# Optimization experiments

Measured on AMD Instinct MI355X. Metric: run time of the kernel, lower is better.

The kernel has to match this reference:

```python
import jax, jax.numpy as jnp
import numpy as np

GRANULARITY = 50
PERCENTILES = (0.01, 0.99)


def setup_inputs() -> dict:
    key = jax.random.key(0)
    H = W = 6144
    sp = jax.random.uniform(key, (H, W), dtype=jnp.float32)
    return {
        "signal_probabilities": sp,
        "rho_max": jnp.float32(H - 1),
        "rho_min": jnp.float32(0.0),
        "theta_min_horizontal": jnp.float32(0.01),
        "theta_max_horizontal": jnp.float32(0.05),
        "theta_min_vertical": jnp.float32(1.52),
        "theta_max_vertical": jnp.float32(1.56),
    }


def _linspace(a, b, n):
    t = jnp.arange(n, dtype=jnp.float32) / (n - 1)
    return a + (b - a) * t


def _fix_edge_effects(buf):
    buf = buf.at[0, :].set(buf[1, :])
    buf = buf.at[-1, :].set(buf[-2, :])
    buf = buf.at[:, 0].set(buf[:, 1])
    buf = buf.at[:, -1].set(buf[:, -2])
    return buf


def _fill_buffer(H, W, thetas, rhos, mode):
    # vectorized over all granularity lines at once (no python loop over lines)
    if mode == "horizontal":
        y = jnp.arange(H)
        # x[g, H]: x = -y*tan(theta) + rho/cos(theta)
        x = -y[None, :] * jnp.tan(thetas)[:, None] + (rhos / jnp.cos(thetas))[:, None]
        x = jnp.clip(jnp.round(x).astype(jnp.int32), 0, W - 1)
        yb = jnp.broadcast_to(y[None, :], x.shape)
        buf = jnp.zeros((H, W), jnp.int32).at[yb, x].add(1)
        buf = jnp.cumsum(buf, axis=1)
    else:
        x = jnp.arange(W)
        # y[g, W]: y = -x/tan(theta) + rho/sin(theta)
        y = -x[None, :] / jnp.tan(thetas)[:, None] + (rhos / jnp.sin(thetas))[:, None]
        y = jnp.clip(jnp.round(y).astype(jnp.int32), 0, H - 1)
        xb = jnp.broadcast_to(x[None, :], y.shape)
        buf = jnp.zeros((H, W), jnp.int32).at[y, xb].add(1)
        buf = jnp.cumsum(buf, axis=0)
    return _fix_edge_effects(buf)


def _get_bounds(nsp, thetas, rhos, mode):
    g = GRANULARITY
    H, W = nsp.shape
    buf = _fill_buffer(H, W, thetas, rhos, mode)
    # segment-sum replaces the dense one_hot * probs reduction (same math)
    values = jax.ops.segment_sum(nsp.reshape(-1), buf.reshape(-1), num_segments=g)
    c = jnp.cumsum(values) / jnp.sum(values)
    lower = jnp.argmax(c >= PERCENTILES[0])  # first index with cumsum >= p0
    upper = (g - 1) - jnp.argmax((c <= PERCENTILES[1])[::-1]) + 2  # last index with cumsum <= p1, +2
    return lower, upper


def _take_neg(a, i):
    # a[-i] with python-style negative indexing (i == 0 -> a[0])
    g = a.shape[0]
    return jnp.take(a, (g - i) % g)


def _intersect(r1, t1, r2, t2):
    det = jnp.cos(t1) * jnp.sin(t2) - jnp.cos(t2) * jnp.sin(t1)
    x = (r1 * jnp.sin(t2) - r2 * jnp.sin(t1)) / det
    y = (r2 * jnp.cos(t1) - r1 * jnp.cos(t2)) / det
    return jnp.stack((x, y))


def reference(signal_probabilities, rho_max, rho_min, theta_min_horizontal,
              theta_max_horizontal, theta_min_vertical, theta_max_vertical):
    g = GRANULARITY
    nsp = signal_probabilities - signal_probabilities.min()
    nsp = nsp / nsp.sum()
    rhos = _linspace(rho_max, rho_min, g)
    th = _linspace(theta_min_horizontal, theta_max_horizontal, g)
    tv = _linspace(theta_min_vertical, theta_max_vertical, g)
    lh, uh = _get_bounds(nsp, th, rhos, "horizontal")
    lv, uv = _get_bounds(nsp, tv, rhos, "vertical")
    r_min_h, r_max_h = _take_neg(rhos, lh), _take_neg(rhos, uh)
    t_min_h, t_max_h = _take_neg(th, lh), _take_neg(th, uh)
    r_min_v, r_max_v = _take_neg(rhos, lv), _take_neg(rhos, uv)
    t_min_v, t_max_v = _take_neg(tv, lv), _take_neg(tv, uv)
    # [top-left, top-right, bottom-right, bottom-left] -> shape (4, 2)
    return jnp.stack([
        _intersect(r_min_h, t_min_h, r_min_v, t_min_v),
        _intersect(r_max_h, t_max_h, r_min_v, t_min_v),
        _intersect(r_max_h, t_max_h, r_max_v, t_max_v),
        _intersect(r_min_h, t_min_h, r_max_v, t_max_v),
    ], axis=0)
```

## Files before the change

kernel.cpp:

```cpp
#include <hip/hip_runtime.h>
#include <math.h>

#define HH 6144
#define WW 6144
constexpr int G = 50;
constexpr int NCOPY = 64;
constexpr int NG = NCOPY * G;
constexpr int BIG = 0x0FFFFFFF;
constexpr int MINBASE = 4 * NG;
constexpr int CTR = MINBASE + NCOPY;
constexpr int MASTER = CTR + NCOPY;
constexpr int C0 = MASTER + 2;

constexpr int TPB  = 384;
constexpr int PXT  = 16;
constexpr int NF4  = WW / 4;
constexpr int NBLK = HH;

__device__ inline void ldsAddF(float* p, float v)      { __hip_atomic_fetch_add(p, v, __ATOMIC_RELAXED, __HIP_MEMORY_SCOPE_WORKGROUP); }
__device__ inline void ldsAddU(unsigned* p, unsigned v){ __hip_atomic_fetch_add(p, v, __ATOMIC_RELAXED, __HIP_MEMORY_SCOPE_WORKGROUP); }
__device__ inline void glbAddF(float* p, float v)      { __hip_atomic_fetch_add(p, v, __ATOMIC_RELAXED, __HIP_MEMORY_SCOPE_AGENT); }
__device__ inline void glbAddU(unsigned* p, unsigned v){ __hip_atomic_fetch_add(p, v, __ATOMIC_RELAXED, __HIP_MEMORY_SCOPE_AGENT); }
__device__ inline unsigned glbAddCtr(unsigned* p)      { return __hip_atomic_fetch_add(p, 1u, __ATOMIC_RELAXED, __HIP_MEMORY_SCOPE_AGENT); }
__device__ inline float atomLoadF(const float* p)      { return __hip_atomic_load(p, __ATOMIC_RELAXED, __HIP_MEMORY_SCOPE_AGENT); }
__device__ inline unsigned atomLoadU(const unsigned* p){ return __hip_atomic_load(p, __ATOMIC_RELAXED, __HIP_MEMORY_SCOPE_AGENT); }

__global__ void crop_init(unsigned int* __restrict__ ws,
                          const float* __restrict__ p_rmax,
                          const float* __restrict__ p_rmin,
                          const float* __restrict__ p_thmin,
                          const float* __restrict__ p_thmax,
                          const float* __restrict__ p_tvmin,
                          const float* __restrict__ p_tvmax) {
  int i = blockIdx.x * 256 + threadIdx.x;
  if (i < MINBASE) ws[i] = 0u;
  else if (i < MINBASE + NCOPY) ws[i] = 0x7F800000u;
  else if (i < C0) ws[i] = 0u;

  if (blockIdx.x == 0 && threadIdx.x < G) {
    int t = threadIdx.x;
    double u    = (double)t / (double)(G - 1);
    double rmax = (double)p_rmax[0], rmin = (double)p_rmin[0];
    double rho  = rmax + (rmin - rmax) * u;
    double th   = (double)p_thmin[0] + ((double)p_thmax[0] - (double)p_thmin[0]) * u;
    double tv   = (double)p_tvmin[0] + ((double)p_tvmax[0] - (double)p_tvmin[0]) * u;
    double cth = cos(th), sth = sin(th);
    double ctv = cos(tv), stv = sin(tv);
    double* dT   = (double*)(ws + C0);
    double* dRC  = (double*)(ws + C0 + 100);
    float*  fva  = (float*)(ws + C0 + 200);
    float*  fvb  = (float*)(ws + C0 + 250);
    double* dRho = (double*)(ws + C0 + 300);
    double* dSth = (double*)(ws + C0 + 400);
    double* dCth = (double*)(ws + C0 + 500);
    double* dStv = (double*)(ws + C0 + 600);
    double* dCtv = (double*)(ws + C0 + 700);
    dT[t]  = tan(th);
    dRC[t] = rho / cth;
    fva[t] = (float)(rho / stv);
    fvb[t] = (float)(ctv / stv);
    dRho[t] = rho; dSth[t] = sth; dCth[t] = cth; dStv[t] = stv; dCtv[t] = ctv;
  }
}

__launch_bounds__(TPB)
__global__ void crop_main(const float* __restrict__ sp,
                          float* __restrict__ wsf,
                          float* __restrict__ out) {
  __shared__ float4 srow[NF4];
  __shared__ int pxh[G], pxv[G];
  __shared__ float hsum[G + 1], vsum[G + 1];
  __shared__ unsigned int hcnt[G + 1], vcnt[G + 1];
  __shared__ float wmin[TPB / 64];
  __shared__ int lastFlag;
  __shared__ double valS[100];
  __shared__ unsigned int valC[100];
  __shared__ float sminv;

  const int t  = threadIdx.x;
  const int y  = blockIdx.x;
  const int yp = min(max(y, 1), HH - 2);
  const float fyp = (float)yp;

  const float4* rowp = (const float4*)(sp + (size_t)y * WW);
  float4 a0 = rowp[t], a1 = rowp[t + 384], a2 = rowp[t + 768], a3 = rowp[t + 1152];

  for (int i = t; i < G + 1; i += TPB) { hsum[i] = 0.f; vsum[i] = 0.f; hcnt[i] = 0u; vcnt[i] = 0u; }

  const unsigned int* wsu = (const unsigned int*)wsf;
  if (t < G) {
    const double* dT  = (const double*)(wsu + C0);
    const double* dRC = (const double*)(wsu + C0 + 100);
    const float*  fva = (const float*)(wsu + C0 + 200);
    const float*  fvb = (const float*)(wsu + C0 + 250);

    double xg = rint(fma(-(double)yp, dT[t], dRC[t]));
    xg = fmin(fmax(xg, 0.0), (double)(WW - 1));
    int xi = (int)xg;
    pxh[t] = (xi <= 1) ? 0 : (xi >= WW - 1 ? BIG : xi);

    float va = fva[t], vb = fvb[t];
    int lo = 1, hi = WW - 1;
    while (lo < hi) {
      int m = (lo + hi) >> 1;
      float yv = rintf(fmaf(-(float)m, vb, va));
      yv = fminf(fmaxf(yv, 0.f), (float)(HH - 1));
      if (yv <= fyp) hi = m; else lo = m + 1;
    }
    pxv[t] = (lo >= WW - 1) ? BIG : (lo == 1 ? 0 : lo);
  }

  srow[(t)        ^ (((t)        >> 3) & 3)] = a0;
  srow[(t + 384)  ^ (((t + 384)  >> 3) & 3)] = a1;
  srow[(t + 768)  ^ (((t + 768)  >> 3) & 3)] = a2;
  srow[(t + 1152) ^ (((t + 1152) >> 3) & 3)] = a3;
  __syncthreads();

  const int swr = (t >> 1) & 3;
  float4 q0 = srow[(4 * t + 0) ^ swr];
  float4 q1 = srow[(4 * t + 1) ^ swr];
  float4 q2 = srow[(4 * t + 2) ^ swr];
  float4 q3 = srow[(4 * t + 3) ^ swr];
  float px[PXT] = { q0.x,q0.y,q0.z,q0.w, q1.x,q1.y,q1.z,q1.w,
                    q2.x,q2.y,q2.z,q2.w, q3.x,q3.y,q3.z,q3.w };

  const int x0 = t * PXT;

  int lo = 0, hi = G;
  while (lo < hi) { int m = (lo + hi) >> 1; if (pxh[m] <= x0) hi = m; else lo = m + 1; }
  const int lbh = lo;
  const int nbh = (lbh > 0) ? pxh[lbh - 1] : BIG;
  const int kh  = min(nbh - x0, PXT);

  lo = 0; hi = G;
  while (lo < hi) { int m = (lo + hi) >> 1; if (pxv[m] <= x0) hi = m; else lo = m + 1; }
  const int lbv = lo;
  const int nbv = (lbv > 0) ? pxv[lbv - 1] : BIG;
  const int kv  = min(nbv - x0, PXT);

  const int sh = G - lbh, sv = G - lbv;

  float S = 0.f, Ah = 0.f, Av = 0.f, mn = 3.4e38f;
#pragma unroll
  for (int k = 0; k < PXT; ++k) {
    float v = px[k];
    mn = fminf(mn, v);
    S += v;
    if (k + 1 == kh) Ah = S;
    if (k + 1 == kv) Av = S;
  }

  ldsAddF(&hsum[sh], Ah); ldsAddU(&hcnt[sh], (unsigned)kh);
  if (kh < PXT) { ldsAddF(&hsum[sh + 1], S - Ah); ldsAddU(&hcnt[sh + 1], (unsigned)(PXT - kh)); }
  ldsAddF(&vsum[sv], Av); ldsAddU(&vcnt[sv], (unsigned)kv);
  if (kv < PXT) { ldsAddF(&vsum[sv + 1], S - Av); ldsAddU(&vcnt[sv + 1], (unsigned)(PXT - kv)); }

  float m = mn;
  for (int off = 32; off; off >>= 1) m = fminf(m, __shfl_down(m, off));
  if ((t & 63) == 0) wmin[t >> 6] = m;
  __syncthreads();

  const int copy = y & (NCOPY - 1);
  unsigned int* wsw = (unsigned int*)wsf;
  if (t == 0) {
    float mm = wmin[0];
    for (int i = 1; i < TPB / 64; ++i) mm = fminf(mm, wmin[i]);
    atomicMin(&wsw[MINBASE + copy], __float_as_uint(mm));
  }
  if (t < G) {
    glbAddF(&wsf[copy * G + t], hsum[t]);
    glbAddU(&wsw[2 * NG + copy * G + t], hcnt[t]);
  } else if (t >= 64 && t < 64 + G) {
    int s = t - 64;
    glbAddF(&wsf[NG + copy * G + s], vsum[s]);
    glbAddU(&wsw[3 * NG + copy * G + s], vcnt[s]);
  }

  __syncthreads();
  if (t == 0) {
    int last = 0;
    unsigned p1 = glbAddCtr(&wsw[CTR + copy]);
    if (p1 == (unsigned)(NBLK / NCOPY - 1)) {
      unsigned p2 = glbAddCtr(&wsw[MASTER]);
      last = (p2 == (unsigned)(NCOPY - 1));
    }
    lastFlag = last;
  }
  __syncthreads();
  if (!lastFlag) return;

  if (t < 64) {
    float v = __uint_as_float(atomLoadU(&wsu[MINBASE + t]));
    for (int off = 32; off; off >>= 1) v = fminf(v, __shfl_down(v, off));
    if (t == 0) sminv = v;
  }
  if (t < 100) {
    const int fam = t >= G;
    const int g = fam ? t - G : t;
    const int sumBase = fam ? NG : 0;
    const int cntBase = (2 + fam) * NG;
    double s = 0.0; unsigned int c = 0;
#pragma unroll 8
    for (int cp = 0; cp < NCOPY; ++cp) {
      s += (double)atomLoadF(&wsf[sumBase + cp * G + g]);
      c += atomLoadU(&wsu[cntBase + cp * G + g]);
    }
    valS[t] = s; valC[t] = c;
  }
  __syncthreads();

  if (t == 0) {
    const double mv = (double)sminv;
    auto bounds = [&](int base, int& lowerI, int& upperI) {
      double tot = 0;
      for (int s = 0; s < G; ++s) tot += valS[base + s] - mv * (double)valC[base + s];
      double c = 0; bool found = false; int last = -1; lowerI = 0;
      for (int s = 0; s < G; ++s) {
        c += valS[base + s] - mv * (double)valC[base + s];
        double cc = c / tot;
        if (!found && cc >= 0.01) { lowerI = s; found = true; }
        if (cc <= 0.99) last = s;
      }
      upperI = (last < 0) ? (G + 1) : (last + 2);
    };
    int lh, uh, lv, uv;
    bounds(0, lh, uh);
    bounds(G, lv, uv);

    const double* dRho = (const double*)(wsu + C0 + 300);
    const double* dSth = (const double*)(wsu + C0 + 400);
    const double* dCth = (const double*)(wsu + C0 + 500);
    const double* dStv = (const double*)(wsu + C0 + 600);
    const double* dCtv = (const double*)(wsu + C0 + 700);

    auto tn = [&](int i) { return ((G - i) % G + G) % G; };
    int ihmin = tn(lh), ihmax = tn(uh), ivmin = tn(lv), ivmax = tn(uv);

    auto inter = [&](int ih, int iv, float* o) {
      double r1 = dRho[ih], s1 = dSth[ih], c1 = dCth[ih];
      double r2 = dRho[iv], s2 = dStv[iv], c2 = dCtv[iv];
      double det = c1 * s2 - c2 * s1;
      o[0] = (float)((r1 * s2 - r2 * s1) / det);
      o[1] = (float)((r2 * c1 - r1 * c2) / det);
    };
    inter(ihmin, ivmin, out + 0);
    inter(ihmax, ivmin, out + 2);
    inter(ihmax, ivmax, out + 4);
    inter(ihmin, ivmax, out + 6);
  }
}

extern "C" void kernel_launch(void* const* d_in, const int* in_sizes, int n_in,
                              void* d_out, int out_size, void* d_ws, size_t ws_size,
                              hipStream_t stream) {
  const float* sp    = (const float*)d_in[0];
  const float* rmax  = (const float*)d_in[1];
  const float* rmin  = (const float*)d_in[2];
  const float* thmin = (const float*)d_in[3];
  const float* thmax = (const float*)d_in[4];
  const float* tvmin = (const float*)d_in[5];
  const float* tvmax = (const float*)d_in[6];
  float* wsf  = (float*)d_ws;
  float* outp = (float*)d_out;

  crop_init<<<(C0 + 255) / 256, 256, 0, stream>>>((unsigned int*)d_ws,
                                                  rmax, rmin, thmin, thmax, tvmin, tvmax);
  crop_main<<<NBLK, TPB, 0, stream>>>(sp, wsf, outp);
}
```

Before: 250.1 us.

## Load row pixels directly per thread and shrink block tail to single wavefront

Each thread now loads its 16 contiguous pixels straight from global memory instead of staging the whole row through a swizzled LDS buffer, which removes the 24KB shared array and one LDS round trip. The block-min reduction uses an LDS atomic min instead of a per-wave array. After the block barrier only the first wavefront continues: it issues all global atomics, waits on vmcnt, and decides last-block status with a shuffle, which removes two block barriers. The direct loads are strided per lane (64B apart), so global coalescing is less clean, and the finaliser relies on a single wavefront with manual waitcnt.

```diff
diff --git a/kernel.cpp b/kernel.cpp
--- a/kernel.cpp
+++ b/kernel.cpp
@@ -14,13 +14,14 @@
 
 constexpr int TPB  = 384;
 constexpr int PXT  = 16;
-constexpr int NF4  = WW / 4;
 constexpr int NBLK = HH;
 
 __device__ inline void ldsAddF(float* p, float v)      { __hip_atomic_fetch_add(p, v, __ATOMIC_RELAXED, __HIP_MEMORY_SCOPE_WORKGROUP); }
 __device__ inline void ldsAddU(unsigned* p, unsigned v){ __hip_atomic_fetch_add(p, v, __ATOMIC_RELAXED, __HIP_MEMORY_SCOPE_WORKGROUP); }
+__device__ inline void ldsMinU(unsigned* p, unsigned v){ __hip_atomic_fetch_min(p, v, __ATOMIC_RELAXED, __HIP_MEMORY_SCOPE_WORKGROUP); }
 __device__ inline void glbAddF(float* p, float v)      { __hip_atomic_fetch_add(p, v, __ATOMIC_RELAXED, __HIP_MEMORY_SCOPE_AGENT); }
 __device__ inline void glbAddU(unsigned* p, unsigned v){ __hip_atomic_fetch_add(p, v, __ATOMIC_RELAXED, __HIP_MEMORY_SCOPE_AGENT); }
+__device__ inline void glbMinU(unsigned* p, unsigned v){ __hip_atomic_fetch_min(p, v, __ATOMIC_RELAXED, __HIP_MEMORY_SCOPE_AGENT); }
 __device__ inline unsigned glbAddCtr(unsigned* p)      { return __hip_atomic_fetch_add(p, 1u, __ATOMIC_RELAXED, __HIP_MEMORY_SCOPE_AGENT); }
 __device__ inline float atomLoadF(const float* p)      { return __hip_atomic_load(p, __ATOMIC_RELAXED, __HIP_MEMORY_SCOPE_AGENT); }
 __device__ inline unsigned atomLoadU(const unsigned* p){ return __hip_atomic_load(p, __ATOMIC_RELAXED, __HIP_MEMORY_SCOPE_AGENT); }
@@ -67,25 +68,23 @@
 __global__ void crop_main(const float* __restrict__ sp,
                           float* __restrict__ wsf,
                           float* __restrict__ out) {
-  __shared__ float4 srow[NF4];
   __shared__ int pxh[G], pxv[G];
   __shared__ float hsum[G + 1], vsum[G + 1];
   __shared__ unsigned int hcnt[G + 1], vcnt[G + 1];
-  __shared__ float wmin[TPB / 64];
-  __shared__ int lastFlag;
-  __shared__ double valS[100];
-  __shared__ unsigned int valC[100];
-  __shared__ float sminv;
+  __shared__ unsigned int blockMinBits;
+  __shared__ double valD[100];
 
   const int t  = threadIdx.x;
   const int y  = blockIdx.x;
   const int yp = min(max(y, 1), HH - 2);
   const float fyp = (float)yp;
-
-  const float4* rowp = (const float4*)(sp + (size_t)y * WW);
-  float4 a0 = rowp[t], a1 = rowp[t + 384], a2 = rowp[t + 768], a3 = rowp[t + 1152];
+  const int x0 = t * PXT;
+
+  const float4* p4 = (const float4*)(sp + (size_t)y * WW + x0);
+  float4 q0 = p4[0], q1 = p4[1], q2 = p4[2], q3 = p4[3];
 
   for (int i = t; i < G + 1; i += TPB) { hsum[i] = 0.f; vsum[i] = 0.f; hcnt[i] = 0u; vcnt[i] = 0u; }
+  if (t == TPB - 1) blockMinBits = 0x7F800000u;
 
   const unsigned int* wsu = (const unsigned int*)wsf;
   if (t < G) {
@@ -109,22 +108,10 @@
     }
     pxv[t] = (lo >= WW - 1) ? BIG : (lo == 1 ? 0 : lo);
   }
-
-  srow[(t)        ^ (((t)        >> 3) & 3)] = a0;
-  srow[(t + 384)  ^ (((t + 384)  >> 3) & 3)] = a1;
-  srow[(t + 768)  ^ (((t + 768)  >> 3) & 3)] = a2;
-  srow[(t + 1152) ^ (((t + 1152) >> 3) & 3)] = a3;
   __syncthreads();
 
-  const int swr = (t >> 1) & 3;
-  float4 q0 = srow[(4 * t + 0) ^ swr];
-  float4 q1 = srow[(4 * t + 1) ^ swr];
-  float4 q2 = srow[(4 * t + 2) ^ swr];
-  float4 q3 = srow[(4 * t + 3) ^ swr];
   float px[PXT] = { q0.x,q0.y,q0.z,q0.w, q1.x,q1.y,q1.z,q1.w,
                     q2.x,q2.y,q2.z,q2.w, q3.x,q3.y,q3.z,q3.w };
-
-  const int x0 = t * PXT;
 
   int lo = 0, hi = G;
   while (lo < hi) { int m = (lo + hi) >> 1; if (pxh[m] <= x0) hi = m; else lo = m + 1; }
@@ -155,73 +142,68 @@
   ldsAddF(&vsum[sv], Av); ldsAddU(&vcnt[sv], (unsigned)kv);
   if (kv < PXT) { ldsAddF(&vsum[sv + 1], S - Av); ldsAddU(&vcnt[sv + 1], (unsigned)(PXT - kv)); }
 
-  float m = mn;
-  for (int off = 32; off; off >>= 1) m = fminf(m, __shfl_down(m, off));
-  if ((t & 63) == 0) wmin[t >> 6] = m;
+  for (int off = 32; off; off >>= 1) mn = fminf(mn, __shfl_down(mn, off));
+  if ((t & 63) == 0) ldsMinU(&blockMinBits, __float_as_uint(mn));
+
   __syncthreads();
+
+  if (t >= 64) return;
 
   const int copy = y & (NCOPY - 1);
   unsigned int* wsw = (unsigned int*)wsf;
-  if (t == 0) {
-    float mm = wmin[0];
-    for (int i = 1; i < TPB / 64; ++i) mm = fminf(mm, wmin[i]);
-    atomicMin(&wsw[MINBASE + copy], __float_as_uint(mm));
-  }
   if (t < G) {
     glbAddF(&wsf[copy * G + t], hsum[t]);
     glbAddU(&wsw[2 * NG + copy * G + t], hcnt[t]);
-  } else if (t >= 64 && t < 64 + G) {
-    int s = t - 64;
-    glbAddF(&wsf[NG + copy * G + s], vsum[s]);
-    glbAddU(&wsw[3 * NG + copy * G + s], vcnt[s]);
-  }
-
-  __syncthreads();
+    glbAddF(&wsf[NG + copy * G + t], vsum[t]);
+    glbAddU(&wsw[3 * NG + copy * G + t], vcnt[t]);
+  }
+  if (t == 0) glbMinU(&wsw[MINBASE + copy], blockMinBits);
+
+  asm volatile("s_waitcnt vmcnt(0)" ::: "memory");
+
+  int last = 0;
   if (t == 0) {
-    int last = 0;
     unsigned p1 = glbAddCtr(&wsw[CTR + copy]);
     if (p1 == (unsigned)(NBLK / NCOPY - 1)) {
       unsigned p2 = glbAddCtr(&wsw[MASTER]);
       last = (p2 == (unsigned)(NCOPY - 1));
     }
-    lastFlag = last;
-  }
-  __syncthreads();
-  if (!lastFlag) return;
-
-  if (t < 64) {
-    float v = __uint_as_float(atomLoadU(&wsu[MINBASE + t]));
-    for (int off = 32; off; off >>= 1) v = fminf(v, __shfl_down(v, off));
-    if (t == 0) sminv = v;
-  }
-  if (t < 100) {
-    const int fam = t >= G;
-    const int g = fam ? t - G : t;
+  }
+  last = __shfl(last, 0);
+  if (!last) return;
+
+  float vmn = __uint_as_float(atomLoadU(&wsu[MINBASE + t]));
+  for (int off = 32; off; off >>= 1) vmn = fminf(vmn, __shfl_down(vmn, off));
+  const double mv = (double)__shfl(vmn, 0);
+
+  for (int p = t; p < 100; p += 64) {
+    const int fam = p >= G;
+    const int g = fam ? p - G : p;
     const int sumBase = fam ? NG : 0;
     const int cntBase = (2 + fam) * NG;
-    double s = 0.0; unsigned int c = 0;
+    double s = 0.0; unsigned c = 0;
 #pragma unroll 8
     for (int cp = 0; cp < NCOPY; ++cp) {
       s += (double)atomLoadF(&wsf[sumBase + cp * G + g]);
       c += atomLoadU(&wsu[cntBase + cp * G + g]);
     }
-    valS[t] = s; valC[t] = c;
-  }
-  __syncthreads();
+    valD[p] = s - mv * (double)c;
+  }
+  asm volatile("s_waitcnt lgkmcnt(0)" ::: "memory");
+  __builtin_amdgcn_sched_barrier(0);
 
   if (t == 0) {
-    const double mv = (double)sminv;
     auto bounds = [&](int base, int& lowerI, int& upperI) {
       double tot = 0;
-      for (int s = 0; s < G; ++s) tot += valS[base + s] - mv * (double)valC[base + s];
-      double c = 0; bool found = false; int last = -1; lowerI = 0;
+      for (int s = 0; s < G; ++s) tot += valD[base + s];
+      double c = 0; bool found = false; int lastI = -1; lowerI = 0;
       for (int s = 0; s < G; ++s) {
-        c += valS[base + s] - mv * (double)valC[base + s];
+        c += valD[base + s];
         double cc = c / tot;
         if (!found && cc >= 0.01) { lowerI = s; found = true; }
-        if (cc <= 0.99) last = s;
+        if (cc <= 0.99) lastI = s;
       }
-      upperI = (last < 0) ? (G + 1) : (last + 2);
+      upperI = (lastI < 0) ? (G + 1) : (lastI + 2);
     };
     int lh, uh, lv, uv;
     bounds(0, lh, uh);
```

After: 251.6 us. Within noise of the previous version (+0.6%).
